# Optimization experiments

Measured on AMD Instinct MI355X. Metric: run time of the kernel, lower is better.

Reference implementation:

```python
import jax, jax.numpy as jnp
import numpy as np

N_NODES = 100000
N_EDGES = 1600000
IN_DIM = 256
OUT_DIM = 128
EPS = 1e-12  # torch F.normalize default eps


def setup_inputs() -> dict:
    key = jax.random.key(0)
    k1, k2, k3, k4, k5 = jax.random.split(key, 5)
    x = jax.random.normal(k1, (N_NODES, IN_DIM), dtype=jnp.float32)
    edge_index = jax.random.randint(k2, (2, N_EDGES), 0, N_NODES, dtype=jnp.int64)
    # projection (no bias): weight [out, in]
    Wp = jax.random.normal(k3, (OUT_DIM, IN_DIM), dtype=jnp.float32) * 0.05
    # GCNConv internal linear weight [out, out] and output bias [out]
    Wg = jax.random.normal(k4, (OUT_DIM, OUT_DIM), dtype=jnp.float32) * 0.05
    bg = jax.random.normal(k5, (OUT_DIM,), dtype=jnp.float32) * 0.01
    return {"x": x, "edge_index": edge_index, "Wp": Wp, "Wg": Wg, "bg": bg}


def reference(x, edge_index, Wp, Wg, bg):
    n = x.shape[0]
    # projection: x @ Wp^T
    h = x @ Wp.T                      # [N, OUT]
    # GCNConv: transform first, then propagate
    h = h @ Wg.T                      # [N, OUT]
    # add self-loops
    loops = jnp.arange(n, dtype=edge_index.dtype)
    row = jnp.concatenate([edge_index[0], loops])   # source
    col = jnp.concatenate([edge_index[1], loops])   # target
    # symmetric normalization: deg over target index (edge_weight = 1)
    deg = jax.ops.segment_sum(jnp.ones_like(col, dtype=h.dtype), col, num_segments=n)
    dinv = jnp.where(deg > 0, jax.lax.rsqrt(deg), 0.0)
    norm = dinv[row] * dinv[col]                     # [E+N]
    # gather messages from source, scale, scatter-add to target
    msg = h[row] * norm[:, None]                     # [E+N, OUT]
    out = jax.ops.segment_sum(msg, col, num_segments=n)  # [N, OUT]
    out = out + bg
    # F.normalize(dim=1): divide by L2 norm clamped at eps
    nrm = jnp.sqrt(jnp.sum(out * out, axis=1, keepdims=True))
    out = out / jnp.maximum(nrm, EPS)
    return out
```

## Files before the change

kernel.cpp:

```cpp
#include <hip/hip_runtime.h>
#include <hip/hip_fp16.h>

#define NDIM 128
#define KDIM 256
#define MT 5
#define AROW 264
#define CHUNK 6400
#define MAXBUCK 128

typedef _Float16 half8 __attribute__((ext_vector_type(8)));
typedef float float4v __attribute__((ext_vector_type(4)));

__global__ void k_combine_w(const float* __restrict__ Wp, const float* __restrict__ Wg,
                            _Float16* __restrict__ Bfrag) {
    int o = blockIdx.x;
    int i = threadIdx.x;
    float acc = 0.f;
#pragma unroll 4
    for (int k = 0; k < 128; ++k) acc = fmaf(Wg[o * 128 + k], Wp[k * 256 + i], acc);
    int kk = i >> 5, r = i & 31, quad = r >> 3, j = r & 7;
    int ntile = o >> 4, lanen = o & 15, lane = quad * 16 + lanen;
    Bfrag[(((ntile * 8 + kk) * 64) + lane) * 8 + j] = (_Float16)acc;
}

__global__ __launch_bounds__(256) void k_phase1(const int* __restrict__ col, int E,
                                                int* __restrict__ hist, int NBLK, int NBUCK) {
    __shared__ int h[MAXBUCK];
    int tid = threadIdx.x;
    if (tid < MAXBUCK) h[tid] = 0;
    __syncthreads();
    int e0 = blockIdx.x * CHUNK;
    int e1 = min(e0 + CHUNK, E);
    for (int e = e0 + tid; e < e1; e += 256) atomicAdd(&h[col[e] >> 10], 1);
    __syncthreads();
    if (tid < NBUCK) hist[tid * NBLK + blockIdx.x] = h[tid];
}

__global__ __launch_bounds__(1024) void k_scan2(int* __restrict__ hist, int NE) {
    __shared__ int s[1024];
    int t = threadIdx.x;
    int CH = (NE + 1023) >> 10;
    int off = t * CH;
    int sum = 0;
    for (int j = 0; j < CH; ++j) { int idx = off + j; if (idx < NE) sum += hist[idx]; }
    s[t] = sum;
    __syncthreads();
    for (int d = 1; d < 1024; d <<= 1) {
        int y = (t >= d) ? s[t - d] : 0;
        __syncthreads();
        s[t] += y;
        __syncthreads();
    }
    int run = s[t] - sum;
    for (int j = 0; j < CH; ++j) {
        int idx = off + j;
        if (idx < NE) { int v = hist[idx]; hist[idx] = run; run += v; }
    }
}

__global__ __launch_bounds__(256) void k_phase3(const int* __restrict__ ei, int E,
                                                const int* __restrict__ offs, int NBLK, int NBUCK,
                                                int2* __restrict__ tmp) {
    __shared__ int cur[MAXBUCK];
    int tid = threadIdx.x;
    if (tid < NBUCK) cur[tid] = offs[tid * NBLK + blockIdx.x];
    __syncthreads();
    int e0 = blockIdx.x * CHUNK;
    int e1 = min(e0 + CHUNK, E);
    for (int e = e0 + tid; e < e1; e += 256) {
        int r = ei[e];
        int c = ei[E + e];
        int p = atomicAdd(&cur[c >> 10], 1);
        tmp[p] = make_int2(r, c);
    }
}

__global__ __launch_bounds__(1024) void k_fine(const int2* __restrict__ tmp,
                                               const int* __restrict__ offs, int NBLK, int NBUCK,
                                               int N, int E,
                                               int* __restrict__ sortedRow,
                                               int* __restrict__ cnt,
                                               int* __restrict__ rowStart) {
    __shared__ int scnt[1024];
    __shared__ int cur[1024];
    int b = blockIdx.x;
    int t = threadIdx.x;
    int nodeBase = b << 10;
    int start = offs[b * NBLK];
    int end = (b + 1 < NBUCK) ? offs[(b + 1) * NBLK] : E;

    scnt[t] = 0;
    __syncthreads();
    for (int p = start + t; p < end; p += 1024) atomicAdd(&scnt[tmp[p].y - nodeBase], 1);
    __syncthreads();
    int v = scnt[t];
    for (int d = 1; d < 1024; d <<= 1) {
        int y = (t >= d) ? scnt[t - d] : 0;
        __syncthreads();
        scnt[t] += y;
        __syncthreads();
    }
    int excl = scnt[t] - v;
    int node = nodeBase + t;
    if (node < N) {
        cnt[node] = v;
        rowStart[node] = start + excl;
    }
    cur[t] = start + excl;
    __syncthreads();
    for (int p = start + t; p < end; p += 1024) {
        int2 pr = tmp[p];
        int slot = atomicAdd(&cur[pr.y - nodeBase], 1);
        sortedRow[slot] = pr.x;
    }
    if (b == NBUCK - 1 && t == 0) rowStart[N] = E;
}

__global__ __launch_bounds__(256) void k_gemm_mfma(const float* __restrict__ x,
                                                   const _Float16* __restrict__ Bfrag,
                                                   const int* __restrict__ cnt,
                                                   _Float16* __restrict__ g, int nrows) {
    __shared__ __align__(16) _Float16 xs[16 * AROW];
    int tid  = threadIdx.x;
    int lane = tid & 63;
    int w    = tid >> 6;
    int quad = lane >> 4;
    int lcol = lane & 15;

    const half8* Bv = (const half8*)Bfrag;
    half8 b0[8], b1[8];
#pragma unroll
    for (int kk = 0; kk < 8; ++kk) {
        b0[kk] = Bv[(w * 8 + kk) * 64 + lane];
        b1[kk] = Bv[((w + 4) * 8 + kk) * 64 + lane];
    }

    long base = (long)blockIdx.x * (16 * MT);
    for (int t = 0; t < MT; ++t) {
        long m0 = base + t * 16;
        __syncthreads();
        const float4* xv = (const float4*)(x + m0 * KDIM);
#pragma unroll
        for (int ii = 0; ii < 4; ++ii) {
            int idx = tid + ii * 256;
            int m = idx >> 6, k4 = idx & 63;
            float4 v = xv[idx];
            _Float16* d = &xs[m * AROW + k4 * 4];
            d[0] = (_Float16)v.x; d[1] = (_Float16)v.y;
            d[2] = (_Float16)v.z; d[3] = (_Float16)v.w;
        }
        __syncthreads();

        float4v acc0 = {0.f, 0.f, 0.f, 0.f}, acc1 = {0.f, 0.f, 0.f, 0.f};
#pragma unroll
        for (int kk = 0; kk < 8; ++kk) {
            half8 a = *(const half8*)(&xs[lcol * AROW + kk * 32 + quad * 8]);
            acc0 = __builtin_amdgcn_mfma_f32_16x16x32_f16(a, b0[kk], acc0, 0, 0, 0);
            acc1 = __builtin_amdgcn_mfma_f32_16x16x32_f16(a, b1[kk], acc1, 0, 0, 0);
        }

#pragma unroll
        for (int r = 0; r < 4; ++r) {
            long node = m0 + quad * 4 + r;
            float di = rsqrtf((float)(cnt[node] + 1));
            g[node * NDIM + w * 16 + lcol]        = (_Float16)(acc0[r] * di);
            g[node * NDIM + (w + 4) * 16 + lcol]  = (_Float16)(acc1[r] * di);
        }
    }
}

__global__ __launch_bounds__(256) void k_gather(const _Float16* __restrict__ g,
                                                const int* __restrict__ rowStart,
                                                const int* __restrict__ sortedRow,
                                                const int* __restrict__ cnt,
                                                const float* __restrict__ bg,
                                                float* __restrict__ out) {
    int lane = threadIdx.x & 63;
    int i = blockIdx.x * 4 + (threadIdx.x >> 6);
    const int s = rowStart[i];
    const int e = rowStart[i + 1];
    const int g4  = lane >> 4;
    const int r16 = lane & 15;

    const half8* __restrict__ gv = (const half8*)g;

    float acc[8];
#pragma unroll
    for (int j = 0; j < 8; ++j) acc[j] = 0.f;

    int p = s;
    for (; p + 16 <= e; p += 16) {
        int r0 = sortedRow[p + g4];
        int r1 = sortedRow[p + 4 + g4];
        int r2 = sortedRow[p + 8 + g4];
        int r3 = sortedRow[p + 12 + g4];
        half8 v0 = gv[(size_t)r0 * 16 + r16];
        half8 v1 = gv[(size_t)r1 * 16 + r16];
        half8 v2 = gv[(size_t)r2 * 16 + r16];
        half8 v3 = gv[(size_t)r3 * 16 + r16];
#pragma unroll
        for (int j = 0; j < 8; ++j)
            acc[j] += ((float)v0[j] + (float)v1[j]) + ((float)v2[j] + (float)v3[j]);
    }
    for (; p + 4 <= e; p += 4) {
        int r0 = sortedRow[p + g4];
        half8 v0 = gv[(size_t)r0 * 16 + r16];
#pragma unroll
        for (int j = 0; j < 8; ++j) acc[j] += (float)v0[j];
    }
    if (p + g4 < e) {
        int r0 = sortedRow[p + g4];
        half8 v0 = gv[(size_t)r0 * 16 + r16];
#pragma unroll
        for (int j = 0; j < 8; ++j) acc[j] += (float)v0[j];
    }

#pragma unroll
    for (int j = 0; j < 8; ++j) {
        acc[j] += __shfl_xor(acc[j], 16);
        acc[j] += __shfl_xor(acc[j], 32);
    }

    half8 sv = gv[(size_t)i * 16 + r16];
#pragma unroll
    for (int j = 0; j < 8; ++j) acc[j] += (float)sv[j];

    float di = rsqrtf((float)(cnt[i] + 1));
    float4 b0 = ((const float4*)bg)[r16 * 2];
    float4 b1 = ((const float4*)bg)[r16 * 2 + 1];
    float v[8];
    v[0] = fmaf(di, acc[0], b0.x);
    v[1] = fmaf(di, acc[1], b0.y);
    v[2] = fmaf(di, acc[2], b0.z);
    v[3] = fmaf(di, acc[3], b0.w);
    v[4] = fmaf(di, acc[4], b1.x);
    v[5] = fmaf(di, acc[5], b1.y);
    v[6] = fmaf(di, acc[6], b1.z);
    v[7] = fmaf(di, acc[7], b1.w);

    float sq = 0.f;
#pragma unroll
    for (int j = 0; j < 8; ++j) sq += v[j] * v[j];
    sq += __shfl_xor(sq, 1);
    sq += __shfl_xor(sq, 2);
    sq += __shfl_xor(sq, 4);
    sq += __shfl_xor(sq, 8);
    float scale = 1.0f / fmaxf(sqrtf(sq), 1e-12f);

    if (g4 == 0) {
        float4 o0 = make_float4(v[0] * scale, v[1] * scale, v[2] * scale, v[3] * scale);
        float4 o1 = make_float4(v[4] * scale, v[5] * scale, v[6] * scale, v[7] * scale);
        ((float4*)out)[(size_t)i * 32 + r16 * 2]     = o0;
        ((float4*)out)[(size_t)i * 32 + r16 * 2 + 1] = o1;
    }
}

extern "C" void kernel_launch(void* const* d_in, const int* in_sizes, int n_in,
                              void* d_out, int out_size, void* d_ws, size_t ws_size,
                              hipStream_t stream) {
    const float* x  = (const float*)d_in[0];
    const int*   ei = (const int*)  d_in[1];
    const float* Wp = (const float*)d_in[2];
    const float* Wg = (const float*)d_in[3];
    const float* bg = (const float*)d_in[4];
    float* out = (float*)d_out;

    const int N = in_sizes[0] / KDIM;
    const int E = in_sizes[1] / 2;

    const int NBLK  = (E + CHUNK - 1) / CHUNK;
    const int NBUCK = (N + 1023) >> 10;
    const int NE    = NBLK * NBUCK;

    char* p = (char*)d_ws;
    auto carve = [&](size_t bytes) { void* r = (void*)p; p += (bytes + 255) & ~(size_t)255; return r; };
    _Float16* g      = (_Float16*)carve((size_t)N * NDIM * 2);
    int*   sortedRow = (int*)  carve((size_t)E * 4);
    int2*  tmp       = (int2*) carve((size_t)E * 8);
    _Float16* Bfrag  = (_Float16*)carve((size_t)KDIM * NDIM * 2);
    int*   cnt       = (int*)  carve((size_t)N * 4);
    int*   rowStart  = (int*)  carve((size_t)(N + 1) * 4);
    int*   hist      = (int*)  carve((size_t)NE * 4);

    hipLaunchKernelGGL(k_combine_w, dim3(NDIM), dim3(KDIM), 0, stream, Wp, Wg, Bfrag);
    hipLaunchKernelGGL(k_phase1, dim3(NBLK), dim3(256), 0, stream, ei + E, E, hist, NBLK, NBUCK);
    hipLaunchKernelGGL(k_scan2, dim3(1), dim3(1024), 0, stream, hist, NE);
    hipLaunchKernelGGL(k_phase3, dim3(NBLK), dim3(256), 0, stream, ei, E, hist, NBLK, NBUCK, tmp);
    hipLaunchKernelGGL(k_fine, dim3(NBUCK), dim3(1024), 0, stream, tmp, hist, NBLK, NBUCK, N, E,
                       sortedRow, cnt, rowStart);
    hipLaunchKernelGGL(k_gemm_mfma, dim3(N / (16 * MT)), dim3(256), 0, stream, x, Bfrag, cnt, g, N);
    hipLaunchKernelGGL(k_gather, dim3(N / 4), dim3(256), 0, stream,
                       g, rowStart, sortedRow, cnt, bg, out);
}
```

Baseline: 353.5 us.

## Parallelize histogram scan, shrink buckets, pack edge pairs, double-buffer GEMM tile

Replaces the single-block serial scan of the bucket histogram with a three-kernel hierarchical scan. It halves bucket width and chunk size for more parallelism in the sort phases. Source and target-low bits are packed into one int, halving temp traffic. The GEMM's LDS staging tile is double-buffered to drop one barrier per iteration, and the stores are vectorized. This adds two kernel launches and relies on node indices fitting in 22 bits.

```diff
diff --git a/kernel.cpp b/kernel.cpp
--- a/kernel.cpp
+++ b/kernel.cpp
@@ -5,10 +5,13 @@
 #define KDIM 256
 #define MT 5
 #define AROW 264
-#define CHUNK 6400
-#define MAXBUCK 128
+#define CHUNK 3200
+#define BSH 9
+#define BMASK 511
+#define MAXBUCK 256
 
 typedef _Float16 half8 __attribute__((ext_vector_type(8)));
+typedef _Float16 half4v __attribute__((ext_vector_type(4)));
 typedef float float4v __attribute__((ext_vector_type(4)));
 
 __global__ void k_combine_w(const float* __restrict__ Wp, const float* __restrict__ Wg,
@@ -27,23 +30,22 @@
                                                 int* __restrict__ hist, int NBLK, int NBUCK) {
     __shared__ int h[MAXBUCK];
     int tid = threadIdx.x;
-    if (tid < MAXBUCK) h[tid] = 0;
+    h[tid] = 0;
     __syncthreads();
     int e0 = blockIdx.x * CHUNK;
     int e1 = min(e0 + CHUNK, E);
-    for (int e = e0 + tid; e < e1; e += 256) atomicAdd(&h[col[e] >> 10], 1);
+    for (int e = e0 + tid; e < e1; e += 256) atomicAdd(&h[col[e] >> BSH], 1);
     __syncthreads();
     if (tid < NBUCK) hist[tid * NBLK + blockIdx.x] = h[tid];
 }
 
-__global__ __launch_bounds__(1024) void k_scan2(int* __restrict__ hist, int NE) {
+__global__ __launch_bounds__(1024) void k_scan_blk(int* __restrict__ a, int n,
+                                                   int* __restrict__ blockSum) {
     __shared__ int s[1024];
     int t = threadIdx.x;
-    int CH = (NE + 1023) >> 10;
-    int off = t * CH;
-    int sum = 0;
-    for (int j = 0; j < CH; ++j) { int idx = off + j; if (idx < NE) sum += hist[idx]; }
-    s[t] = sum;
+    int i = blockIdx.x * 1024 + t;
+    int v = (i < n) ? a[i] : 0;
+    s[t] = v;
     __syncthreads();
     for (int d = 1; d < 1024; d <<= 1) {
         int y = (t >= d) ? s[t - d] : 0;
@@ -51,16 +53,34 @@
         s[t] += y;
         __syncthreads();
     }
-    int run = s[t] - sum;
-    for (int j = 0; j < CH; ++j) {
-        int idx = off + j;
-        if (idx < NE) { int v = hist[idx]; hist[idx] = run; run += v; }
-    }
+    if (i < n) a[i] = s[t] - v;
+    if (t == 1023) blockSum[blockIdx.x] = s[t];
+}
+
+__global__ __launch_bounds__(1024) void k_scan_top(int* __restrict__ blockSum, int nb) {
+    __shared__ int s[1024];
+    int t = threadIdx.x;
+    int v = (t < nb) ? blockSum[t] : 0;
+    s[t] = v;
+    __syncthreads();
+    for (int d = 1; d < 1024; d <<= 1) {
+        int y = (t >= d) ? s[t - d] : 0;
+        __syncthreads();
+        s[t] += y;
+        __syncthreads();
+    }
+    if (t < nb) blockSum[t] = s[t] - v;
+}
+
+__global__ __launch_bounds__(256) void k_scan_add(int* __restrict__ a,
+                                                  const int* __restrict__ blockOff, int n) {
+    int i = blockIdx.x * 256 + threadIdx.x;
+    if (i < n) a[i] += blockOff[i >> 10];
 }
 
 __global__ __launch_bounds__(256) void k_phase3(const int* __restrict__ ei, int E,
                                                 const int* __restrict__ offs, int NBLK, int NBUCK,
-                                                int2* __restrict__ tmp) {
+                                                int* __restrict__ tmp) {
     __shared__ int cur[MAXBUCK];
     int tid = threadIdx.x;
     if (tid < NBUCK) cur[tid] = offs[tid * NBLK + blockIdx.x];
@@ -70,48 +90,47 @@
     for (int e = e0 + tid; e < e1; e += 256) {
         int r = ei[e];
         int c = ei[E + e];
-        int p = atomicAdd(&cur[c >> 10], 1);
-        tmp[p] = make_int2(r, c);
-    }
-}
-
-__global__ __launch_bounds__(1024) void k_fine(const int2* __restrict__ tmp,
-                                               const int* __restrict__ offs, int NBLK, int NBUCK,
-                                               int N, int E,
-                                               int* __restrict__ sortedRow,
-                                               int* __restrict__ cnt,
-                                               int* __restrict__ rowStart) {
-    __shared__ int scnt[1024];
-    __shared__ int cur[1024];
+        int p = atomicAdd(&cur[c >> BSH], 1);
+        tmp[p] = (r << BSH) | (c & BMASK);
+    }
+}
+
+__global__ __launch_bounds__(512) void k_fine(const int* __restrict__ tmp,
+                                              const int* __restrict__ offs, int NBLK, int NBUCK,
+                                              int N, int E,
+                                              int* __restrict__ sortedRow,
+                                              int* __restrict__ cnt,
+                                              int* __restrict__ rowStart) {
+    __shared__ int scnt[512];
+    __shared__ int cur[512];
     int b = blockIdx.x;
     int t = threadIdx.x;
-    int nodeBase = b << 10;
     int start = offs[b * NBLK];
     int end = (b + 1 < NBUCK) ? offs[(b + 1) * NBLK] : E;
 
     scnt[t] = 0;
     __syncthreads();
-    for (int p = start + t; p < end; p += 1024) atomicAdd(&scnt[tmp[p].y - nodeBase], 1);
+    for (int p = start + t; p < end; p += 512) atomicAdd(&scnt[tmp[p] & BMASK], 1);
     __syncthreads();
     int v = scnt[t];
-    for (int d = 1; d < 1024; d <<= 1) {
+    for (int d = 1; d < 512; d <<= 1) {
         int y = (t >= d) ? scnt[t - d] : 0;
         __syncthreads();
         scnt[t] += y;
         __syncthreads();
     }
     int excl = scnt[t] - v;
-    int node = nodeBase + t;
+    int node = (b << BSH) + t;
     if (node < N) {
         cnt[node] = v;
         rowStart[node] = start + excl;
     }
     cur[t] = start + excl;
     __syncthreads();
-    for (int p = start + t; p < end; p += 1024) {
-        int2 pr = tmp[p];
-        int slot = atomicAdd(&cur[pr.y - nodeBase], 1);
-        sortedRow[slot] = pr.x;
+    for (int p = start + t; p < end; p += 512) {
+        int pr = tmp[p];
+        int slot = atomicAdd(&cur[pr & BMASK], 1);
+        sortedRow[slot] = pr >> BSH;
     }
     if (b == NBUCK - 1 && t == 0) rowStart[N] = E;
 }
@@ -120,7 +139,7 @@
                                                    const _Float16* __restrict__ Bfrag,
                                                    const int* __restrict__ cnt,
                                                    _Float16* __restrict__ g, int nrows) {
-    __shared__ __align__(16) _Float16 xs[16 * AROW];
+    __shared__ __align__(16) _Float16 xs[2][16 * AROW];
     int tid  = threadIdx.x;
     int lane = tid & 63;
     int w    = tid >> 6;
@@ -138,23 +157,22 @@
     long base = (long)blockIdx.x * (16 * MT);
     for (int t = 0; t < MT; ++t) {
         long m0 = base + t * 16;
-        __syncthreads();
+        _Float16* xb = xs[t & 1];
         const float4* xv = (const float4*)(x + m0 * KDIM);
 #pragma unroll
         for (int ii = 0; ii < 4; ++ii) {
             int idx = tid + ii * 256;
             int m = idx >> 6, k4 = idx & 63;
             float4 v = xv[idx];
-            _Float16* d = &xs[m * AROW + k4 * 4];
-            d[0] = (_Float16)v.x; d[1] = (_Float16)v.y;
-            d[2] = (_Float16)v.z; d[3] = (_Float16)v.w;
+            half4v hv = { (_Float16)v.x, (_Float16)v.y, (_Float16)v.z, (_Float16)v.w };
+            *(half4v*)&xb[m * AROW + k4 * 4] = hv;
         }
         __syncthreads();
 
         float4v acc0 = {0.f, 0.f, 0.f, 0.f}, acc1 = {0.f, 0.f, 0.f, 0.f};
 #pragma unroll
         for (int kk = 0; kk < 8; ++kk) {
-            half8 a = *(const half8*)(&xs[lcol * AROW + kk * 32 + quad * 8]);
+            half8 a = *(const half8*)(&xb[lcol * AROW + kk * 32 + quad * 8]);
             acc0 = __builtin_amdgcn_mfma_f32_16x16x32_f16(a, b0[kk], acc0, 0, 0, 0);
             acc1 = __builtin_amdgcn_mfma_f32_16x16x32_f16(a, b1[kk], acc1, 0, 0, 0);
         }
@@ -269,24 +287,28 @@
     const int E = in_sizes[1] / 2;
 
     const int NBLK  = (E + CHUNK - 1) / CHUNK;
-    const int NBUCK = (N + 1023) >> 10;
+    const int NBUCK = (N + BMASK) >> BSH;
     const int NE    = NBLK * NBUCK;
+    const int NSB   = (NE + 1023) >> 10;
 
     char* p = (char*)d_ws;
     auto carve = [&](size_t bytes) { void* r = (void*)p; p += (bytes + 255) & ~(size_t)255; return r; };
     _Float16* g      = (_Float16*)carve((size_t)N * NDIM * 2);
     int*   sortedRow = (int*)  carve((size_t)E * 4);
-    int2*  tmp       = (int2*) carve((size_t)E * 8);
+    int*   tmp       = (int*)  carve((size_t)E * 4);
     _Float16* Bfrag  = (_Float16*)carve((size_t)KDIM * NDIM * 2);
     int*   cnt       = (int*)  carve((size_t)N * 4);
     int*   rowStart  = (int*)  carve((size_t)(N + 1) * 4);
     int*   hist      = (int*)  carve((size_t)NE * 4);
+    int*   blockSum  = (int*)  carve((size_t)1024 * 4);
 
     hipLaunchKernelGGL(k_combine_w, dim3(NDIM), dim3(KDIM), 0, stream, Wp, Wg, Bfrag);
     hipLaunchKernelGGL(k_phase1, dim3(NBLK), dim3(256), 0, stream, ei + E, E, hist, NBLK, NBUCK);
-    hipLaunchKernelGGL(k_scan2, dim3(1), dim3(1024), 0, stream, hist, NE);
+    hipLaunchKernelGGL(k_scan_blk, dim3(NSB), dim3(1024), 0, stream, hist, NE, blockSum);
+    hipLaunchKernelGGL(k_scan_top, dim3(1), dim3(1024), 0, stream, blockSum, NSB);
+    hipLaunchKernelGGL(k_scan_add, dim3((NE + 255) / 256), dim3(256), 0, stream, hist, blockSum, NE);
     hipLaunchKernelGGL(k_phase3, dim3(NBLK), dim3(256), 0, stream, ei, E, hist, NBLK, NBUCK, tmp);
-    hipLaunchKernelGGL(k_fine, dim3(NBUCK), dim3(1024), 0, stream, tmp, hist, NBLK, NBUCK, N, E,
+    hipLaunchKernelGGL(k_fine, dim3(NBUCK), dim3(512), 0, stream, tmp, hist, NBLK, NBUCK, N, E,
                        sortedRow, cnt, rowStart);
     hipLaunchKernelGGL(k_gemm_mfma, dim3(N / (16 * MT)), dim3(256), 0, stream, x, Bfrag, cnt, g, N);
     hipLaunchKernelGGL(k_gather, dim3(N / 4), dim3(256), 0, stream,
```

After: 307.3 us. 1.15x faster.
